# Performance work log

Measured on AMD Instinct MI355X. Metric: run time of the kernel, lower is better.

## Reference

```python
import jax, jax.numpy as jnp
import numpy as np

N, D, E, B, NMAX, C = 50000, 64, 800000, 50, 1000, 100


def setup_inputs() -> dict:
    key = jax.random.key(0)
    ks = jax.random.split(key, 12)
    s = 0.05
    return {
        "x": jax.random.normal(ks[0], (N, D), jnp.float32),
        "e": jax.random.normal(ks[1], (E, D), jnp.float32),
        "edge_index": jax.random.randint(ks[2], (2, E), 0, N),
        "attr1": jax.random.normal(ks[3], (B, C, D), jnp.float32),
        "nc1": jax.random.uniform(ks[4], (B, NMAX, C), jnp.float32),
        "x_idx": jnp.arange(N),
        "eps1": jnp.zeros((1,), jnp.float32),
        "eps2": jnp.zeros((1,), jnp.float32),
        "W_ma": jax.random.normal(ks[5], (2 * D, D), jnp.float32) * s,
        "b_ma": jnp.zeros((D,), jnp.float32),
        "W_mu": jax.random.normal(ks[6], (D, D), jnp.float32) * s,
        "b_mu": jnp.zeros((D,), jnp.float32),
        "W_ua": jax.random.normal(ks[7], (D, D), jnp.float32) * s,
        "b_ua": jnp.zeros((D,), jnp.float32),
        "W_uu": jax.random.normal(ks[8], (D, D), jnp.float32) * s,
        "b_uu": jnp.zeros((D,), jnp.float32),
        "W_c": jax.random.normal(ks[9], (2 * D, D), jnp.float32) * s,
        "b_c": jnp.zeros((D,), jnp.float32),
    }


def reference(x, e, edge_index, attr1, nc1, x_idx, eps1, eps2,
              W_ma, b_ma, W_mu, b_mu, W_ua, b_ua, W_uu, b_uu, W_c, b_c):
    # adjacency branch: gather -> MLP -> scatter-sum (GIN-style)
    x_j = x[edge_index[0]]                                   # [E, D]
    msg_adj = jax.nn.relu(jnp.concatenate([x_j, e], axis=-1) @ W_ma + b_ma)
    agg_adj = jax.ops.segment_sum(msg_adj, edge_index[1], num_segments=x.shape[0])
    # hierarchical pooling branch: cluster MLP then dense matmul back to nodes
    msg_up = jax.nn.relu(attr1 @ W_mu + b_mu)                # [B, C, D]
    agg_up = jnp.einsum('bnc,bcd->bnd', nc1, msg_up)         # [B, NMAX, D]
    agg_up = agg_up.reshape(-1, agg_up.shape[-1])[x_idx]     # [N, D]
    out_adj = jax.nn.relu((agg_adj + (1.0 + eps1) * x) @ W_ua + b_ua)
    out_up = jax.nn.relu((agg_up + (1.0 + eps2) * x) @ W_uu + b_uu)
    return jnp.concatenate([out_adj, out_up], axis=-1) @ W_c + b_c
```

## Files before the change

kernel.cpp:

```cpp
#include <hip/hip_runtime.h>

#define NN 50000
#define DD 64
#define EE 800000
#define BB 50
#define NMAXX 1000
#define CC 100

typedef short short8 __attribute__((ext_vector_type(8)));
typedef float float4v __attribute__((ext_vector_type(4)));

__device__ __forceinline__ float rl(float v, int l) {
  return __int_as_float(__builtin_amdgcn_readlane(__float_as_int(v), l));
}
__device__ __forceinline__ short f2bf(float f) {
  unsigned u = __float_as_uint(f);
  unsigned r = (u + 0x7fffu + ((u >> 16) & 1u)) >> 16;
  return (short)r;
}
__device__ __forceinline__ unsigned pack2(float a, float b) {
  return (unsigned)(unsigned short)f2bf(a) |
         ((unsigned)(unsigned short)f2bf(b) << 16);
}
__device__ __forceinline__ short8 pack8(const float* p) {
  union { unsigned u[4]; short8 s; } r;
  float4 v0 = *(const float4*)p;
  float4 v1 = *(const float4*)(p + 4);
  r.u[0] = pack2(v0.x, v0.y); r.u[1] = pack2(v0.z, v0.w);
  r.u[2] = pack2(v1.x, v1.y); r.u[3] = pack2(v1.z, v1.w);
  return r.s;
}


__global__ __launch_bounds__(256) void k_prep(
    const int* __restrict__ ei, const float* __restrict__ x,
    const float* __restrict__ Wma, const float* __restrict__ Wua,
    const float* __restrict__ Wuu, const float* __restrict__ Wc,
    int* __restrict__ cnt, short* __restrict__ xb,
    short* __restrict__ WtF, short* __restrict__ WtF1,
    short* __restrict__ WtF2, short* __restrict__ WtF3) {
  const int i = blockIdx.x * 256 + threadIdx.x;
  if (i < EE) atomicAdd(&cnt[ei[EE + i]], 1);
  if (i < NN * 64) xb[i] = f2bf(x[i]);
  if (i < 8192) {
    int j = i & 7, lane = (i >> 3) & 63, cbks = i >> 9;
    int cb = cbks & 3, ks = cbks >> 2;
    int k = ks * 32 + (lane >> 4) * 8 + j;
    int n = cb * 16 + (lane & 15);
    WtF[i]  = f2bf(Wma[k * 64 + n]);
    WtF3[i] = f2bf(Wc[k * 64 + n]);
    if (i < 4096) {
      WtF1[i] = f2bf(Wua[k * 64 + n]);
      WtF2[i] = f2bf(Wuu[k * 64 + n]);
    }
  }
}

#define CHUNK 196
__global__ __launch_bounds__(256) void k_scan1(const int* __restrict__ cnt,
                                               int* __restrict__ part) {
  __shared__ int s[256];
  const int t = threadIdx.x, b = blockIdx.x;
  const int gi = b * CHUNK + t;
  s[t] = (t < CHUNK && gi < NN) ? cnt[gi] : 0;
  __syncthreads();
#pragma unroll
  for (int off = 128; off; off >>= 1) {
    if (t < off) s[t] += s[t + off];
    __syncthreads();
  }
  if (t == 0) part[b] = s[0];
}
__global__ __launch_bounds__(256) void k_scan2(const int* __restrict__ part,
                                               int* __restrict__ partx) {
  if (threadIdx.x == 0) {
    int r = 0;
    for (int i = 0; i < 256; ++i) { partx[i] = r; r += part[i]; }
  }
}
__global__ __launch_bounds__(256) void k_scan3(const int* __restrict__ cnt,
                                               const int* __restrict__ partx,
                                               int* __restrict__ head) {
  __shared__ int s[256];
  const int t = threadIdx.x, b = blockIdx.x;
  const int gi = b * CHUNK + t;
  int v = (t < CHUNK && gi < NN) ? cnt[gi] : 0;
  s[t] = v;
  __syncthreads();
#pragma unroll
  for (int off = 1; off < 256; off <<= 1) {
    int tv = (t >= off) ? s[t - off] : 0;
    __syncthreads();
    s[t] += tv;
    __syncthreads();
  }
  if (t < CHUNK && gi < NN) head[gi] = partx[b] + s[t] - v;
}

__global__ __launch_bounds__(256) void k_scatter(
    const int* __restrict__ ei, int* __restrict__ head,
    int* __restrict__ srcS, int* __restrict__ dstS, int* __restrict__ perm) {
  const int q = blockIdx.x * 256 + threadIdx.x;
  int d = ei[EE + q];
  int pos = atomicAdd(&head[d], 1);
  srcS[pos] = ei[q];
  dstS[pos] = d;
  perm[pos] = q;
}

__global__ __launch_bounds__(256) void k_msgup(
    const float* __restrict__ attr1, const float* __restrict__ Wmu,
    const float* __restrict__ bmu, short* __restrict__ msgupT) {
  __shared__ float Wl[64 * 64];
  const int tid = threadIdx.x;
  for (int i = tid; i < 64 * 64; i += 256) Wl[i] = Wmu[i];
  __syncthreads();
  const int lane = tid & 63;
  const int row = blockIdx.x * 4 + (tid >> 6);
  float a = attr1[(size_t)row * 64 + lane];
  float acc = bmu[lane];
#pragma unroll 8
  for (int k = 0; k < 64; ++k)
    acc = fmaf(rl(a, k), Wl[k * 64 + lane], acc);
  const int b = row / 100, c = row - b * 100;
  msgupT[(size_t)b * 6400 + lane * 100 + c] = f2bf(fmaxf(acc, 0.f));
}

__global__ __launch_bounds__(256) void k_aggup(
    const float* __restrict__ nc1, const short* __restrict__ msgupT,
    float* __restrict__ aggup) {
  constexpr int LDA = 136;
  __shared__ float Ncf[64 * CC];
  __shared__ short A[64 * LDA];
  __shared__ short Wt[64 * LDA];
  const int b = blockIdx.x >> 4;
  const int tile = blockIdx.x & 15;
  const int i0 = tile * 64;
  const int tid = threadIdx.x;
  const float* ncb = nc1 + ((size_t)b * NMAXX + i0) * CC;
  for (int idx = tid; idx < 64 * CC; idx += 256) {
    int r = idx / CC;
    Ncf[idx] = (i0 + r < NMAXX) ? ncb[idx] : 0.f;
  }
  {
    const unsigned* src = (const unsigned*)(msgupT + (size_t)b * 6400);
    unsigned* dstw = (unsigned*)Wt;
    for (int i = tid; i < 64 * 50; i += 256) {
      int row = i / 50, cu = i - row * 50;
      dstw[row * 68 + cu] = src[i];
    }
    for (int i = tid; i < 64 * 14; i += 256) {
      int row = i / 14, cu = 50 + (i - row * 14);
      dstw[row * 68 + cu] = 0;
    }
  }
  __syncthreads();
  {
    const int row = tid >> 2, kp = tid & 3;
#pragma unroll
    for (int j = 0; j < 16; ++j) {
      int k = kp * 32 + 2 * j;
      unsigned u = 0;
      if (k < CC) {
        float2 v = *(const float2*)&Ncf[row * CC + k];
        u = pack2(v.x, v.y);
      }
      *(unsigned*)&A[row * LDA + k] = u;
    }
  }
  __syncthreads();
  const int lane = tid & 63;
  const int w = tid >> 6;
  const int m = lane & 15;
  const int koff = (lane >> 4) * 8;
  float4v acc[4];
#pragma unroll
  for (int cb = 0; cb < 4; ++cb) acc[cb] = (float4v)0.f;
#pragma unroll
  for (int ks = 0; ks < 4; ++ks) {
    short8 af = *(const short8*)&A[(w * 16 + m) * LDA + ks * 32 + koff];
#pragma unroll
    for (int cb = 0; cb < 4; ++cb) {
      short8 bf = *(const short8*)&Wt[(cb * 16 + m) * LDA + ks * 32 + koff];
      acc[cb] = __builtin_amdgcn_mfma_f32_16x16x32_bf16(af, bf, acc[cb], 0, 0, 0);
    }
  }
  const int rbase = (lane >> 4) * 4;
#pragma unroll
  for (int cb = 0; cb < 4; ++cb)
#pragma unroll
    for (int r = 0; r < 4; ++r) {
      int i = i0 + w * 16 + rbase + r;
      if (i < NMAXX)
        aggup[((size_t)b * NMAXX + i) * 64 + cb * 16 + m] = acc[cb][r];
    }
}

__global__ __launch_bounds__(256) void k_edge_mfma(
    const short* __restrict__ xb, const float* __restrict__ e,
    const int* __restrict__ perm, const int* __restrict__ srcS,
    const int* __restrict__ dstSg, const short* __restrict__ WtF,
    const float* __restrict__ bma, float* __restrict__ agg) {
  __shared__ short WtL[8192];
  __shared__ float Cs[4][16][68];
  const int tid = threadIdx.x;
  {
    const uint4* s = (const uint4*)WtF;
    uint4* d = (uint4*)WtL;
#pragma unroll
    for (int it = 0; it < 4; ++it) d[it * 256 + tid] = s[it * 256 + tid];
  }
  __syncthreads();
  const int lane = tid & 63;
  const int wv = tid >> 6;
  const int m = lane & 15;
  const int koff = (lane >> 4) * 8;
  float bias[4];
#pragma unroll
  for (int cb = 0; cb < 4; ++cb) bias[cb] = bma[cb * 16 + m];
  const int p00 = blockIdx.x * 128;
#pragma unroll
  for (int half = 0; half < 2; ++half) {
    const int tb = p00 + (half * 4 + wv) * 16;
    const int p = tb + m;
    const int src = srcS[p];
    const int eid = perm[p];
    short8 a0 = *(const short8*)(xb + (size_t)src * 64 + koff);
    short8 a1 = *(const short8*)(xb + (size_t)src * 64 + 32 + koff);
    const float* er = e + (size_t)eid * 64;
    short8 a2 = pack8(er + koff);
    short8 a3 = pack8(er + 32 + koff);
    float4v acc[4];
#pragma unroll
    for (int cb = 0; cb < 4; ++cb) acc[cb] = (float4v)0.f;
#pragma unroll
    for (int cb = 0; cb < 4; ++cb) {
      short8 b0 = *(const short8*)&WtL[((0 * 4 + cb) * 64 + lane) * 8];
      short8 b1 = *(const short8*)&WtL[((1 * 4 + cb) * 64 + lane) * 8];
      short8 b2 = *(const short8*)&WtL[((2 * 4 + cb) * 64 + lane) * 8];
      short8 b3 = *(const short8*)&WtL[((3 * 4 + cb) * 64 + lane) * 8];
      acc[cb] = __builtin_amdgcn_mfma_f32_16x16x32_bf16(a0, b0, acc[cb], 0, 0, 0);
      acc[cb] = __builtin_amdgcn_mfma_f32_16x16x32_bf16(a1, b1, acc[cb], 0, 0, 0);
      acc[cb] = __builtin_amdgcn_mfma_f32_16x16x32_bf16(a2, b2, acc[cb], 0, 0, 0);
      acc[cb] = __builtin_amdgcn_mfma_f32_16x16x32_bf16(a3, b3, acc[cb], 0, 0, 0);
    }
    const int rbase = (lane >> 4) * 4;
#pragma unroll
    for (int cb = 0; cb < 4; ++cb)
#pragma unroll
      for (int r = 0; r < 4; ++r)
        Cs[wv][rbase + r][cb * 16 + m] = fmaxf(acc[cb][r] + bias[cb], 0.f);
    int dseg[16];
#pragma unroll
    for (int r = 0; r < 16; ++r) dseg[r] = dstSg[tb + r];
    int dprev = -1;
    float run = 0.f;
#pragma unroll
    for (int r = 0; r < 16; ++r) {
      float v = Cs[wv][r][lane];
      if (dseg[r] != dprev) {
        if (run != 0.f) atomicAdd(&agg[(size_t)dprev * 64 + lane], run);
        run = 0.f;
        dprev = dseg[r];
      }
      run += v;
    }
    if (run != 0.f) atomicAdd(&agg[(size_t)dprev * 64 + lane], run);
  }
}

__global__ __launch_bounds__(256) void k_final(
    const float* __restrict__ x, const float* __restrict__ agg,
    const float* __restrict__ aggup, const int* __restrict__ xidx,
    const float* __restrict__ eps1, const float* __restrict__ eps2,
    const short* __restrict__ WtF1, const float* __restrict__ bua,
    const short* __restrict__ WtF2, const float* __restrict__ buu,
    const short* __restrict__ WtF3, const float* __restrict__ bc,
    float* __restrict__ out) {
  constexpr int LD1 = 72;
  constexpr int LD3 = 136;
  __shared__ short A1[64 * LD1];
  __shared__ short A2[64 * LD1];
  __shared__ short O[64 * LD3];
  const int tid = threadIdx.x;
  const float s1 = 1.f + eps1[0], s2 = 1.f + eps2[0];
  const int r0 = blockIdx.x * 64;
  {
    const int row = tid >> 2, kp = tid & 3;
    int g = r0 + row;
    if (g >= NN) g = NN - 1;
    const size_t xb_ = (size_t)g * 64 + kp * 16;
    const size_t ub = (size_t)xidx[g] * 64 + kp * 16;
#pragma unroll
    for (int j = 0; j < 4; ++j) {
      float4 xv = *(const float4*)&x[xb_ + j * 4];
      float4 av = *(const float4*)&agg[xb_ + j * 4];
      float4 uv = *(const float4*)&aggup[ub + j * 4];
      unsigned h1lo = pack2(av.x + s1 * xv.x, av.y + s1 * xv.y);
      unsigned h1hi = pack2(av.z + s1 * xv.z, av.w + s1 * xv.w);
      unsigned h2lo = pack2(uv.x + s2 * xv.x, uv.y + s2 * xv.y);
      unsigned h2hi = pack2(uv.z + s2 * xv.z, uv.w + s2 * xv.w);
      *(uint2*)&A1[row * LD1 + kp * 16 + j * 4] = make_uint2(h1lo, h1hi);
      *(uint2*)&A2[row * LD1 + kp * 16 + j * 4] = make_uint2(h2lo, h2hi);
    }
  }
  __syncthreads();
  const int lane = tid & 63;
  const int w = tid >> 6;
  const int m = lane & 15;
  const int koff = (lane >> 4) * 8;
  const int rbase = (lane >> 4) * 4;
  float4v acc1[4], acc2[4];
#pragma unroll
  for (int cb = 0; cb < 4; ++cb) { acc1[cb] = (float4v)0.f; acc2[cb] = (float4v)0.f; }
#pragma unroll
  for (int ks = 0; ks < 2; ++ks) {
    short8 a1 = *(const short8*)&A1[(w * 16 + m) * LD1 + ks * 32 + koff];
    short8 a2 = *(const short8*)&A2[(w * 16 + m) * LD1 + ks * 32 + koff];
#pragma unroll
    for (int cb = 0; cb < 4; ++cb) {
      short8 b1 = *(const short8*)&WtF1[((ks * 4 + cb) * 64 + lane) * 8];
      short8 b2 = *(const short8*)&WtF2[((ks * 4 + cb) * 64 + lane) * 8];
      acc1[cb] = __builtin_amdgcn_mfma_f32_16x16x32_bf16(a1, b1, acc1[cb], 0, 0, 0);
      acc2[cb] = __builtin_amdgcn_mfma_f32_16x16x32_bf16(a2, b2, acc2[cb], 0, 0, 0);
    }
  }
#pragma unroll
  for (int cb = 0; cb < 4; ++cb) {
    float bb1 = bua[cb * 16 + m];
    float bb2 = buu[cb * 16 + m];
#pragma unroll
    for (int r = 0; r < 4; ++r) {
      int rowL = w * 16 + rbase + r;
      O[rowL * LD3 + cb * 16 + m] = f2bf(fmaxf(acc1[cb][r] + bb1, 0.f));
      O[rowL * LD3 + 64 + cb * 16 + m] = f2bf(fmaxf(acc2[cb][r] + bb2, 0.f));
    }
  }
  __syncthreads();
  float4v acc3[4];
#pragma unroll
  for (int cb = 0; cb < 4; ++cb) acc3[cb] = (float4v)0.f;
#pragma unroll
  for (int ks = 0; ks < 4; ++ks) {
    short8 af = *(const short8*)&O[(w * 16 + m) * LD3 + ks * 32 + koff];
#pragma unroll
    for (int cb = 0; cb < 4; ++cb) {
      short8 bf = *(const short8*)&WtF3[((ks * 4 + cb) * 64 + lane) * 8];
      acc3[cb] = __builtin_amdgcn_mfma_f32_16x16x32_bf16(af, bf, acc3[cb], 0, 0, 0);
    }
  }
#pragma unroll
  for (int cb = 0; cb < 4; ++cb) {
    float bb = bc[cb * 16 + m];
#pragma unroll
    for (int r = 0; r < 4; ++r) {
      int g = r0 + w * 16 + rbase + r;
      if (g < NN)
        out[(size_t)g * 64 + cb * 16 + m] = acc3[cb][r] + bb;
    }
  }
}

extern "C" void kernel_launch(void* const* d_in, const int* in_sizes, int n_in,
                              void* d_out, int out_size, void* d_ws, size_t ws_size,
                              hipStream_t stream) {
  const float* x     = (const float*)d_in[0];
  const float* e     = (const float*)d_in[1];
  const int*   ei    = (const int*)d_in[2];
  const float* attr1 = (const float*)d_in[3];
  const float* nc1   = (const float*)d_in[4];
  const int*   xidx  = (const int*)d_in[5];
  const float* eps1  = (const float*)d_in[6];
  const float* eps2  = (const float*)d_in[7];
  const float* Wma   = (const float*)d_in[8];
  const float* bma   = (const float*)d_in[9];
  const float* Wmu   = (const float*)d_in[10];
  const float* bmu   = (const float*)d_in[11];
  const float* Wua   = (const float*)d_in[12];
  const float* bua   = (const float*)d_in[13];
  const float* Wuu   = (const float*)d_in[14];
  const float* buu   = (const float*)d_in[15];
  const float* Wc    = (const float*)d_in[16];
  const float* bc    = (const float*)d_in[17];
  float* out = (float*)d_out;

  float* agg    = (float*)d_ws;
  int*   cnt    = (int*)(agg + (size_t)NN * 64);
  float* aggup  = (float*)(cnt + NN);
  short* msgupT = (short*)(aggup + (size_t)NN * 64);
  short* xbuf   = msgupT + (size_t)BB * 6400;
  int*   head   = (int*)(xbuf + (size_t)NN * 64);
  int*   part   = head + NN;
  int*   partx  = part + 256;
  int*   srcS   = partx + 256;
  int*   dstS   = srcS + EE;
  int*   perm   = dstS + EE;
  short* WtF    = (short*)(perm + EE);
  short* WtF1   = WtF + 8192;
  short* WtF2   = WtF1 + 4096;
  short* WtF3   = WtF2 + 4096;

  hipMemsetAsync(agg, 0, (size_t)NN * 64 * sizeof(float) + NN * sizeof(int),
                 stream);
  k_prep<<<dim3((NN * 64 + 255) / 256), dim3(256), 0, stream>>>(
      ei, x, Wma, Wua, Wuu, Wc, cnt, xbuf, WtF, WtF1, WtF2, WtF3);
  k_scan1<<<dim3(256), dim3(256), 0, stream>>>(cnt, part);
  k_scan2<<<dim3(1), dim3(256), 0, stream>>>(part, partx);
  k_scan3<<<dim3(256), dim3(256), 0, stream>>>(cnt, partx, head);
  k_scatter<<<dim3(EE / 256), dim3(256), 0, stream>>>(ei, head, srcS, dstS, perm);
  k_msgup<<<dim3(BB * CC / 4), dim3(256), 0, stream>>>(attr1, Wmu, bmu, msgupT);
  k_aggup<<<dim3(BB * 16), dim3(256), 0, stream>>>(nc1, msgupT, aggup);
  k_edge_mfma<<<dim3(EE / 128), dim3(256), 0, stream>>>(
      xbuf, e, perm, srcS, dstS, WtF, bma, agg);
  k_final<<<dim3((NN + 63) / 64), dim3(256), 0, stream>>>(
      x, agg, aggup, xidx, eps1, eps2, WtF1, bua, WtF2, buu, WtF3, bc, out);
}
```

Before: 528.8 us.

## Pack sorted edge arrays, widen edge tiles, swizzle blocks per XCD, vectorise prep

Sorted src, dst and edge-id arrays are merged into one packed uint2 per edge, with src and dst in 16-bit halves, cutting index traffic. The edge kernel now processes 64 edges per wave with a running segment sum carried across sub-tiles, which reduces atomic adds. Blocks are remapped so contiguous ranges land on the same XCD for better L2 locality. The x to bf16 conversion is vectorised and the single-thread partial scan becomes a parallel block scan. The 16-bit packing relies on N fitting in 16 bits.

```diff
diff --git a/kernel.cpp b/kernel.cpp
--- a/kernel.cpp
+++ b/kernel.cpp
@@ -40,8 +40,11 @@
     short* __restrict__ WtF, short* __restrict__ WtF1,
     short* __restrict__ WtF2, short* __restrict__ WtF3) {
   const int i = blockIdx.x * 256 + threadIdx.x;
-  if (i < EE) atomicAdd(&cnt[ei[EE + i]], 1);
-  if (i < NN * 64) xb[i] = f2bf(x[i]);
+  atomicAdd(&cnt[ei[EE + i]], 1);
+  {
+    float4 xv = *(const float4*)&x[(size_t)i * 4];
+    ((uint2*)xb)[i] = make_uint2(pack2(xv.x, xv.y), pack2(xv.z, xv.w));
+  }
   if (i < 8192) {
     int j = i & 7, lane = (i >> 3) & 63, cbks = i >> 9;
     int cb = cbks & 3, ks = cbks >> 2;
@@ -73,10 +76,19 @@
 }
 __global__ __launch_bounds__(256) void k_scan2(const int* __restrict__ part,
                                                int* __restrict__ partx) {
-  if (threadIdx.x == 0) {
-    int r = 0;
-    for (int i = 0; i < 256; ++i) { partx[i] = r; r += part[i]; }
-  }
+  __shared__ int s[256];
+  const int t = threadIdx.x;
+  int v = part[t];
+  s[t] = v;
+  __syncthreads();
+#pragma unroll
+  for (int off = 1; off < 256; off <<= 1) {
+    int tv = (t >= off) ? s[t - off] : 0;
+    __syncthreads();
+    s[t] += tv;
+    __syncthreads();
+  }
+  partx[t] = s[t] - v;
 }
 __global__ __launch_bounds__(256) void k_scan3(const int* __restrict__ cnt,
                                                const int* __restrict__ partx,
@@ -99,13 +111,11 @@
 
 __global__ __launch_bounds__(256) void k_scatter(
     const int* __restrict__ ei, int* __restrict__ head,
-    int* __restrict__ srcS, int* __restrict__ dstS, int* __restrict__ perm) {
+    uint2* __restrict__ sde) {
   const int q = blockIdx.x * 256 + threadIdx.x;
   int d = ei[EE + q];
   int pos = atomicAdd(&head[d], 1);
-  srcS[pos] = ei[q];
-  dstS[pos] = d;
-  perm[pos] = q;
+  sde[pos] = make_uint2((unsigned)ei[q] | ((unsigned)d << 16), (unsigned)q);
 }
 
 __global__ __launch_bounds__(256) void k_msgup(
@@ -198,12 +208,15 @@
 
 __global__ __launch_bounds__(256) void k_edge_mfma(
     const short* __restrict__ xb, const float* __restrict__ e,
-    const int* __restrict__ perm, const int* __restrict__ srcS,
-    const int* __restrict__ dstSg, const short* __restrict__ WtF,
+    const uint2* __restrict__ sde, const short* __restrict__ WtF,
     const float* __restrict__ bma, float* __restrict__ agg) {
   __shared__ short WtL[8192];
   __shared__ float Cs[4][16][68];
   const int tid = threadIdx.x;
+  const int nwg = gridDim.x;
+  const int qq = nwg >> 3, rr = nwg & 7;
+  const int xx = blockIdx.x & 7, oo = blockIdx.x >> 3;
+  const int bid = (xx < rr ? xx * (qq + 1) : rr * (qq + 1) + (xx - rr) * qq) + oo;
   {
     const uint4* s = (const uint4*)WtF;
     uint4* d = (uint4*)WtL;
@@ -218,13 +231,16 @@
   float bias[4];
 #pragma unroll
   for (int cb = 0; cb < 4; ++cb) bias[cb] = bma[cb * 16 + m];
-  const int p00 = blockIdx.x * 128;
-#pragma unroll
-  for (int half = 0; half < 2; ++half) {
-    const int tb = p00 + (half * 4 + wv) * 16;
-    const int p = tb + m;
-    const int src = srcS[p];
-    const int eid = perm[p];
+  const int base = bid * 256 + wv * 64;
+  int dprev = -1;
+  float run = 0.f;
+#pragma unroll
+  for (int c4 = 0; c4 < 4; ++c4) {
+    const int tb = base + c4 * 16;
+    const uint2 v = sde[tb + m];
+    const int src = (int)(v.x & 0xffffu);
+    const int dst = (int)(v.x >> 16);
+    const int eid = (int)v.y;
     short8 a0 = *(const short8*)(xb + (size_t)src * 64 + koff);
     short8 a1 = *(const short8*)(xb + (size_t)src * 64 + 32 + koff);
     const float* er = e + (size_t)eid * 64;
@@ -250,23 +266,19 @@
 #pragma unroll
       for (int r = 0; r < 4; ++r)
         Cs[wv][rbase + r][cb * 16 + m] = fmaxf(acc[cb][r] + bias[cb], 0.f);
-    int dseg[16];
-#pragma unroll
-    for (int r = 0; r < 16; ++r) dseg[r] = dstSg[tb + r];
-    int dprev = -1;
-    float run = 0.f;
 #pragma unroll
     for (int r = 0; r < 16; ++r) {
-      float v = Cs[wv][r][lane];
-      if (dseg[r] != dprev) {
+      int dr = __builtin_amdgcn_readlane(dst, r);
+      float val = Cs[wv][r][lane];
+      if (dr != dprev) {
         if (run != 0.f) atomicAdd(&agg[(size_t)dprev * 64 + lane], run);
         run = 0.f;
-        dprev = dseg[r];
+        dprev = dr;
       }
-      run += v;
-    }
-    if (run != 0.f) atomicAdd(&agg[(size_t)dprev * 64 + lane], run);
-  }
+      run += val;
+    }
+  }
+  if (run != 0.f) atomicAdd(&agg[(size_t)dprev * 64 + lane], run);
 }
 
 __global__ __launch_bounds__(256) void k_final(
@@ -392,26 +404,24 @@
   int*   head   = (int*)(xbuf + (size_t)NN * 64);
   int*   part   = head + NN;
   int*   partx  = part + 256;
-  int*   srcS   = partx + 256;
-  int*   dstS   = srcS + EE;
-  int*   perm   = dstS + EE;
-  short* WtF    = (short*)(perm + EE);
+  uint2* sde    = (uint2*)(partx + 256);
+  short* WtF    = (short*)(sde + EE);
   short* WtF1   = WtF + 8192;
   short* WtF2   = WtF1 + 4096;
   short* WtF3   = WtF2 + 4096;
 
   hipMemsetAsync(agg, 0, (size_t)NN * 64 * sizeof(float) + NN * sizeof(int),
                  stream);
-  k_prep<<<dim3((NN * 64 + 255) / 256), dim3(256), 0, stream>>>(
+  k_prep<<<dim3(EE / 256), dim3(256), 0, stream>>>(
       ei, x, Wma, Wua, Wuu, Wc, cnt, xbuf, WtF, WtF1, WtF2, WtF3);
   k_scan1<<<dim3(256), dim3(256), 0, stream>>>(cnt, part);
   k_scan2<<<dim3(1), dim3(256), 0, stream>>>(part, partx);
   k_scan3<<<dim3(256), dim3(256), 0, stream>>>(cnt, partx, head);
-  k_scatter<<<dim3(EE / 256), dim3(256), 0, stream>>>(ei, head, srcS, dstS, perm);
+  k_scatter<<<dim3(EE / 256), dim3(256), 0, stream>>>(ei, head, sde);
   k_msgup<<<dim3(BB * CC / 4), dim3(256), 0, stream>>>(attr1, Wmu, bmu, msgupT);
   k_aggup<<<dim3(BB * 16), dim3(256), 0, stream>>>(nc1, msgupT, aggup);
-  k_edge_mfma<<<dim3(EE / 128), dim3(256), 0, stream>>>(
-      xbuf, e, perm, srcS, dstS, WtF, bma, agg);
+  k_edge_mfma<<<dim3(EE / 256), dim3(256), 0, stream>>>(
+      xbuf, e, sde, WtF, bma, agg);
   k_final<<<dim3((NN + 63) / 64), dim3(256), 0, stream>>>(
       x, agg, aggup, xidx, eps1, eps2, WtF1, bua, WtF2, buu, WtF3, bc, out);
 }
```

Result: faster. 500.4 us (-5.4%).
